# Kernel optimization log

Hardware: AMD Instinct MI355X
Metric: run time of the kernel (lower is better)

Reference implementation:

```python
import jax, jax.numpy as jnp
import numpy as np

TOP_K = 2


def setup_inputs() -> dict:
    key = jax.random.key(0)
    k1, k2, k3, k4 = jax.random.split(key, 4)
    B, S, D, F, E = 4, 512, 512, 2048, 16
    hidden_states = jax.random.normal(k1, (B, S, D), dtype=jnp.float32)
    gate_weight = jax.random.normal(k2, (E, D), dtype=jnp.float32) * 0.02
    w1 = jax.random.normal(k3, (E, F, D), dtype=jnp.float32) * 0.02
    w2 = jax.random.normal(k4, (E, D, F), dtype=jnp.float32) * 0.02
    return {"hidden_states": hidden_states, "gate_weight": gate_weight, "w1": w1, "w2": w2}


def reference(hidden_states, gate_weight, w1, w2):
    B, S, D = hidden_states.shape
    E = gate_weight.shape[0]
    x = hidden_states.reshape(-1, D)  # [T, D]

    # fused_top_k_routing: logits = x @ Wg^T, top-k, softmax over the k values
    gate_logits = x @ gate_weight.T  # [T, E]
    top_vals, top_idx = jax.lax.top_k(gate_logits, TOP_K)  # [T, k]
    routing_w = jax.nn.softmax(top_vals, axis=-1)  # [T, k]

    # _prepare_expert_inputs: token t goes to expert e iff e in its top-k
    mask = jnp.any(top_idx[:, :, None] == jnp.arange(E)[None, None, :], axis=1)  # [T, E] bool

    # Expert FFN on routed tokens, computed densely over (token, expert) pairs then masked.
    # h[t,e,f] = silu(x_t @ W1_e^T)
    h = jax.nn.silu(jnp.einsum('td,efd->tef', x, w1))  # [T, E, F]
    counts = jnp.sum(mask, axis=0)  # [E]
    h_sum = jnp.einsum('tef,te->ef', h, mask.astype(h.dtype))  # [E, F]
    h_mean = h_sum / jnp.maximum(counts, 1)[:, None].astype(h.dtype)

    # fused_expert_scatter_gather uses expert_outputs[e].mean(dim=0);
    # mean(W2 @ act) = W2 @ mean(act) since W2 is linear.
    y_mean = jnp.einsum('ef,edf->ed', h_mean, w2)  # [E, D]
    y_mean = jnp.where((counts > 0)[:, None], y_mean, 0.0)

    # per-token combine: sum_k w_k * mean_output[expert_k]
    out = jnp.einsum('tk,tkd->td', routing_w, y_mean[top_idx])  # [T, D]
    return out.reshape(B, S, D)
```

## Files before the change

kernel.cpp:

```cpp
#include <hip/hip_runtime.h>

#define NTOK   2048
#define DIM    512
#define FDIM   2048
#define NEXP   16
#define CAP    768
#define BT2    128
#define NTB    (CAP / BT2)
#define CNTS   32

typedef __bf16 bf16x8 __attribute__((ext_vector_type(8)));
typedef __bf16 bf16x4 __attribute__((ext_vector_type(4)));
typedef float  floatx4 __attribute__((ext_vector_type(4)));

#define WS_COUNTS    0
#define WS_ZEROPAGE  2048
#define WS_TOPIDX    4096
#define WS_ROUTW     20480
#define WS_HMEAN     36864
#define WS_YMEAN     167936
#define WS_XG        200704
#define WS_ZERO_BYTES 3072

__global__ __launch_bounds__(256) void k1_route_gather(
    const float* __restrict__ x, const float* __restrict__ gw,
    int* __restrict__ counts, int* __restrict__ top_idx,
    float* __restrict__ routw, __bf16* __restrict__ Xg,
    float* __restrict__ hmean)
{
    __shared__ float xt[8 * DIM];
    __shared__ float lg[8][17];
    __shared__ int   cnt_loc[16], base_loc[16];
    __shared__ int   ei[8][2], rk[8][2], gdst[8][2];
    const int tid = threadIdx.x;
    const int t0  = blockIdx.x * 8;

    if (tid < 128) hmean[blockIdx.x * 128 + tid] = 0.f;
    if (tid < 16)  cnt_loc[tid] = 0;

    {
        const float4* src = (const float4*)(x + (size_t)t0 * DIM);
        float4* dst = (float4*)xt;
        #pragma unroll
        for (int i = 0; i < 4; ++i) dst[i * 256 + tid] = src[i * 256 + tid];
    }
    __syncthreads();

    if (tid < 128) {
        const int tl = tid >> 4, e = tid & 15;
        const float4* xr = (const float4*)(xt + tl * DIM);
        const float4* gr = (const float4*)(gw + e * DIM);
        float acc = 0.f;
        #pragma unroll 8
        for (int j = 0; j < DIM / 4; ++j) {
            float4 a = xr[j], b = gr[j];
            acc += a.x * b.x + a.y * b.y + a.z * b.z + a.w * b.w;
        }
        lg[tl][e] = acc;
    }
    __syncthreads();

    if (tid < 8) {
        const int tl = tid;
        float v0 = -1e30f, v1 = -1e30f; int i0 = 0, i1 = 0;
        #pragma unroll
        for (int e = 0; e < NEXP; ++e) {
            float v = lg[tl][e];
            if (v > v0)      { v1 = v0; i1 = i0; v0 = v; i0 = e; }
            else if (v > v1) { v1 = v;  i1 = e; }
        }
        float e1 = __expf(v1 - v0);
        float w0 = 1.f / (1.f + e1);
        float w1 = 1.f - w0;
        const int t = t0 + tl;
        top_idx[t * 2]     = i0; top_idx[t * 2 + 1] = i1;
        routw[t * 2]       = w0; routw[t * 2 + 1]   = w1;
        ei[tl][0] = i0; ei[tl][1] = i1;
        rk[tl][0] = atomicAdd(&cnt_loc[i0], 1);
        rk[tl][1] = atomicAdd(&cnt_loc[i1], 1);
    }
    __syncthreads();
    if (tid < 16) {
        int n = cnt_loc[tid];
        base_loc[tid] = (n > 0) ? atomicAdd(counts + tid * CNTS, n) : 0;
    }
    __syncthreads();
    if (tid < 8) {
        #pragma unroll
        for (int k = 0; k < 2; ++k) {
            int p = base_loc[ei[tid][k]] + rk[tid][k];
            gdst[tid][k] = (p < CAP) ? (ei[tid][k] * CAP + p) : -1;
        }
    }
    __syncthreads();

    #pragma unroll
    for (int it = 0; it < 4; ++it) {
        int s   = it * 256 + tid;
        int job = s >> 6, el = s & 63;
        int tl  = job >> 1, k = job & 1;
        int dst = gdst[tl][k];
        if (dst >= 0) {
            float4 a = ((const float4*)(xt + tl * DIM))[el * 2];
            float4 b = ((const float4*)(xt + tl * DIM))[el * 2 + 1];
            bf16x8 o;
            o[0] = (__bf16)a.x; o[1] = (__bf16)a.y; o[2] = (__bf16)a.z; o[3] = (__bf16)a.w;
            o[4] = (__bf16)b.x; o[5] = (__bf16)b.y; o[6] = (__bf16)b.z; o[7] = (__bf16)b.w;
            *(bf16x8*)(Xg + (size_t)dst * DIM + el * 8) = o;
        }
    }
}

__global__ __launch_bounds__(256) void k2_expert_ffn(
    const float* __restrict__ w1, const __bf16* __restrict__ Xg,
    const int* __restrict__ counts, const __bf16* __restrict__ zp,
    float* __restrict__ hmean)
{
    __shared__ __align__(16) __bf16 w1s[8 * 65 * 8];
    __shared__ __align__(16) __bf16 xs[8 * 129 * 8];
    __shared__ float hred[64][2];

    const int tid = threadIdx.x;
    const int bid = blockIdx.x;
    const int tb  = bid >> 9;
    const int rem = bid & 511;
    const int e   = rem & 15;
    const int f0  = (rem >> 4) * 64;
    const int cnt = min(counts[e * CNTS], CAP);
    if (tb * BT2 >= cnt) return;
    const float inv = 1.f / (float)cnt;

    const int wv   = tid >> 6;
    const int lane = tid & 63;
    const int q    = lane >> 4;
    const int l15  = lane & 15;
    const int fsub = (wv & 1) * 32;
    const int tsub = (wv >> 1) * 64;

    floatx4 acc[2][4];
    #pragma unroll
    for (int a = 0; a < 2; ++a)
        #pragma unroll
        for (int b = 0; b < 4; ++b) acc[a][b] = (floatx4)0.f;

    for (int c = 0; c < 8; ++c) {
        const int d0 = c * 64;
        __syncthreads();
        #pragma unroll
        for (int it = 0; it < 2; ++it) {
            int s = it * 256 + tid;
            int f = s >> 3, g = s & 7;
            const float* src = w1 + ((size_t)(e * FDIM + f0 + f)) * DIM + d0 + g * 8;
            float4 a = ((const float4*)src)[0];
            float4 b = ((const float4*)src)[1];
            bf16x8 v;
            v[0] = (__bf16)a.x; v[1] = (__bf16)a.y; v[2] = (__bf16)a.z; v[3] = (__bf16)a.w;
            v[4] = (__bf16)b.x; v[5] = (__bf16)b.y; v[6] = (__bf16)b.z; v[7] = (__bf16)b.w;
            *(bf16x8*)(w1s + ((size_t)g * 65 + f) * 8) = v;
        }
        {
            const int kg = tid & 7;
            const int r0 = tid >> 3;
            #pragma unroll
            for (int it = 0; it < 4; ++it) {
                int t = it * 32 + r0;
                int r = tb * BT2 + t;
                const __bf16* src = (r < cnt)
                    ? (Xg + ((size_t)(e * CAP + r)) * DIM + d0 + kg * 8)
                    : zp;
                uint4 d = *(const uint4*)src;
                *(uint4*)(xs + ((size_t)kg * 129 + t) * 8) = d;
            }
        }
        __syncthreads();
        #pragma unroll
        for (int ks = 0; ks < 2; ++ks) {
            const int kg = ks * 4 + q;
            bf16x8 af0 = *(const bf16x8*)(w1s + (kg * 65 + fsub + l15) * 8);
            bf16x8 af1 = *(const bf16x8*)(w1s + (kg * 65 + fsub + 16 + l15) * 8);
            #pragma unroll
            for (int tt = 0; tt < 4; ++tt) {
                bf16x8 bfr = *(const bf16x8*)(xs + (kg * 129 + tsub + tt * 16 + l15) * 8);
                acc[0][tt] = __builtin_amdgcn_mfma_f32_16x16x32_bf16(af0, bfr, acc[0][tt], 0, 0, 0);
                acc[1][tt] = __builtin_amdgcn_mfma_f32_16x16x32_bf16(af1, bfr, acc[1][tt], 0, 0, 0);
            }
        }
    }

    float hs[8];
    #pragma unroll
    for (int i = 0; i < 8; ++i) hs[i] = 0.f;
    #pragma unroll
    for (int fa = 0; fa < 2; ++fa)
        #pragma unroll
        for (int tt = 0; tt < 4; ++tt)
            #pragma unroll
            for (int r = 0; r < 4; ++r) {
                float v = acc[fa][tt][r];
                hs[fa * 4 + r] += v / (1.f + __expf(-v));
            }

    #pragma unroll
    for (int i = 0; i < 8; ++i) {
        float v = hs[i];
        v += __shfl_xor(v, 1);
        v += __shfl_xor(v, 2);
        v += __shfl_xor(v, 4);
        v += __shfl_xor(v, 8);
        hs[i] = v;
    }
    if (l15 == 0) {
        #pragma unroll
        for (int fa = 0; fa < 2; ++fa)
            #pragma unroll
            for (int r = 0; r < 4; ++r) {
                int row = fsub + fa * 16 + q * 4 + r;
                hred[row][wv >> 1] = hs[fa * 4 + r];
            }
    }
    __syncthreads();
    if (tid < 64)
        atomicAdd(hmean + (size_t)e * FDIM + f0 + tid,
                  (hred[tid][0] + hred[tid][1]) * inv);
}

__global__ __launch_bounds__(256) void k3_ymean(
    const float* __restrict__ w2, const float* __restrict__ hmean,
    const int* __restrict__ counts, float* __restrict__ ymean)
{
    __shared__ float hl[FDIM];
    const int tid = threadIdx.x;
    const int bid = blockIdx.x;
    const int e   = bid >> 7;
    const int d0  = (bid & 127) * 4;

    {
        const float4* hg = (const float4*)(hmean + (size_t)e * FDIM);
        float4* hl4 = (float4*)hl;
        hl4[tid]       = hg[tid];
        hl4[256 + tid] = hg[256 + tid];
    }
    __syncthreads();

    const int wv = tid >> 6, lane = tid & 63;
    const int d = d0 + wv;
    const float4* wr  = (const float4*)(w2 + ((size_t)e * DIM + d) * FDIM);
    const float4* hl4 = (const float4*)hl;
    float acc = 0.f;
    #pragma unroll
    for (int i = 0; i < 8; ++i) {
        float4 a = wr[i * 64 + lane];
        float4 h = hl4[i * 64 + lane];
        acc += a.x * h.x + a.y * h.y + a.z * h.z + a.w * h.w;
    }
    #pragma unroll
    for (int m = 1; m < 64; m <<= 1) acc += __shfl_xor(acc, m);
    if (lane == 0)
        ymean[e * DIM + d] = (counts[e * CNTS] > 0) ? acc : 0.f;
}

__global__ __launch_bounds__(256) void k4_combine(
    const int* __restrict__ top_idx, const float* __restrict__ routw,
    const float* __restrict__ ymean, float* __restrict__ out)
{
    const int idx = blockIdx.x * 256 + threadIdx.x;
    const int t = idx >> 7;
    const int c = idx & 127;
    const int i0 = top_idx[t * 2], i1 = top_idx[t * 2 + 1];
    const float w0 = routw[t * 2], w1 = routw[t * 2 + 1];
    float4 a = ((const float4*)(ymean + (size_t)i0 * DIM))[c];
    float4 b = ((const float4*)(ymean + (size_t)i1 * DIM))[c];
    float4 o;
    o.x = w0 * a.x + w1 * b.x;
    o.y = w0 * a.y + w1 * b.y;
    o.z = w0 * a.z + w1 * b.z;
    o.w = w0 * a.w + w1 * b.w;
    ((float4*)out)[idx] = o;
}

extern "C" void kernel_launch(void* const* d_in, const int* in_sizes, int n_in,
                              void* d_out, int out_size, void* d_ws, size_t ws_size,
                              hipStream_t stream)
{
    (void)in_sizes; (void)n_in; (void)out_size; (void)ws_size;
    const float* x  = (const float*)d_in[0];
    const float* gw = (const float*)d_in[1];
    const float* w1 = (const float*)d_in[2];
    const float* w2 = (const float*)d_in[3];
    float* out = (float*)d_out;

    char* ws = (char*)d_ws;
    int*    counts  = (int*)   (ws + WS_COUNTS);
    const __bf16* zp = (const __bf16*)(ws + WS_ZEROPAGE);
    int*    top_idx = (int*)   (ws + WS_TOPIDX);
    float*  routw   = (float*) (ws + WS_ROUTW);
    float*  hmean   = (float*) (ws + WS_HMEAN);
    float*  ymean   = (float*) (ws + WS_YMEAN);
    __bf16* Xg      = (__bf16*)(ws + WS_XG);

    hipMemsetAsync(d_ws, 0, WS_ZERO_BYTES, stream);

    k1_route_gather<<<dim3(NTOK / 8), dim3(256), 0, stream>>>(x, gw, counts, top_idx, routw, Xg, hmean);
    k2_expert_ffn  <<<dim3(NTB * 32 * NEXP), dim3(256), 0, stream>>>(w1, Xg, counts, zp, hmean);
    k3_ymean       <<<dim3(NEXP * 128), dim3(256), 0, stream>>>(w2, hmean, counts, ymean);
    k4_combine     <<<dim3(NTOK * DIM / 4 / 256), dim3(256), 0, stream>>>(top_idx, routw, ymean, out);
}
```

Measured before the change: 198.6 us.

## Fuse four MoE kernels into one persistent kernel with grid barriers

Merges routing/gather, expert FFN, W2 projection and combine into a single 512-block persistent kernel separated by software grid barriers on a workspace counter. Each FFN block now loops over all token tiles of its expert and writes hmean directly, so the atomics and the separate hmean zeroing go away. This removes three kernel launch gaps and inter-kernel drains. In exchange it relies on all 512 blocks being co-resident (two per CU) and serializes token tiles per block, which cuts the FFN stage's parallelism.

```diff
diff --git a/kernel.cpp b/kernel.cpp
--- a/kernel.cpp
+++ b/kernel.cpp
@@ -6,14 +6,14 @@
 #define NEXP   16
 #define CAP    768
 #define BT2    128
-#define NTB    (CAP / BT2)
 #define CNTS   32
+#define NBLK   512
 
 typedef __bf16 bf16x8 __attribute__((ext_vector_type(8)));
-typedef __bf16 bf16x4 __attribute__((ext_vector_type(4)));
 typedef float  floatx4 __attribute__((ext_vector_type(4)));
 
 #define WS_COUNTS    0
+#define WS_BAR       64
 #define WS_ZEROPAGE  2048
 #define WS_TOPIDX    4096
 #define WS_ROUTW     20480
@@ -22,260 +22,271 @@
 #define WS_XG        200704
 #define WS_ZERO_BYTES 3072
 
-__global__ __launch_bounds__(256) void k1_route_gather(
+__device__ __forceinline__ void grid_bar(int* bar, int target) {
+    __syncthreads();
+    if (threadIdx.x == 0) {
+        __threadfence();
+        __hip_atomic_fetch_add(bar, 1, __ATOMIC_RELEASE, __HIP_MEMORY_SCOPE_AGENT);
+        while (__hip_atomic_load(bar, __ATOMIC_ACQUIRE, __HIP_MEMORY_SCOPE_AGENT) < target)
+            __builtin_amdgcn_s_sleep(2);
+    }
+    __syncthreads();
+    __threadfence();
+}
+
+__global__ __launch_bounds__(256, 2) void fused_moe(
     const float* __restrict__ x, const float* __restrict__ gw,
-    int* __restrict__ counts, int* __restrict__ top_idx,
-    float* __restrict__ routw, __bf16* __restrict__ Xg,
-    float* __restrict__ hmean)
+    const float* __restrict__ w1, const float* __restrict__ w2,
+    int* counts, int* bar, int* top_idx, float* routw, __bf16* Xg,
+    const __bf16* zp, float* hmean, float* ymean, float* out)
 {
-    __shared__ float xt[8 * DIM];
-    __shared__ float lg[8][17];
-    __shared__ int   cnt_loc[16], base_loc[16];
-    __shared__ int   ei[8][2], rk[8][2], gdst[8][2];
-    const int tid = threadIdx.x;
-    const int t0  = blockIdx.x * 8;
-
-    if (tid < 128) hmean[blockIdx.x * 128 + tid] = 0.f;
-    if (tid < 16)  cnt_loc[tid] = 0;
-
-    {
-        const float4* src = (const float4*)(x + (size_t)t0 * DIM);
-        float4* dst = (float4*)xt;
-        #pragma unroll
-        for (int i = 0; i < 4; ++i) dst[i * 256 + tid] = src[i * 256 + tid];
-    }
-    __syncthreads();
-
-    if (tid < 128) {
-        const int tl = tid >> 4, e = tid & 15;
-        const float4* xr = (const float4*)(xt + tl * DIM);
-        const float4* gr = (const float4*)(gw + e * DIM);
-        float acc = 0.f;
-        #pragma unroll 8
-        for (int j = 0; j < DIM / 4; ++j) {
-            float4 a = xr[j], b = gr[j];
-            acc += a.x * b.x + a.y * b.y + a.z * b.z + a.w * b.w;
-        }
-        lg[tl][e] = acc;
-    }
-    __syncthreads();
-
-    if (tid < 8) {
-        const int tl = tid;
-        float v0 = -1e30f, v1 = -1e30f; int i0 = 0, i1 = 0;
-        #pragma unroll
-        for (int e = 0; e < NEXP; ++e) {
-            float v = lg[tl][e];
-            if (v > v0)      { v1 = v0; i1 = i0; v0 = v; i0 = e; }
-            else if (v > v1) { v1 = v;  i1 = e; }
-        }
-        float e1 = __expf(v1 - v0);
-        float w0 = 1.f / (1.f + e1);
-        float w1 = 1.f - w0;
-        const int t = t0 + tl;
-        top_idx[t * 2]     = i0; top_idx[t * 2 + 1] = i1;
-        routw[t * 2]       = w0; routw[t * 2 + 1]   = w1;
-        ei[tl][0] = i0; ei[tl][1] = i1;
-        rk[tl][0] = atomicAdd(&cnt_loc[i0], 1);
-        rk[tl][1] = atomicAdd(&cnt_loc[i1], 1);
-    }
-    __syncthreads();
-    if (tid < 16) {
-        int n = cnt_loc[tid];
-        base_loc[tid] = (n > 0) ? atomicAdd(counts + tid * CNTS, n) : 0;
-    }
-    __syncthreads();
-    if (tid < 8) {
-        #pragma unroll
-        for (int k = 0; k < 2; ++k) {
-            int p = base_loc[ei[tid][k]] + rk[tid][k];
-            gdst[tid][k] = (p < CAP) ? (ei[tid][k] * CAP + p) : -1;
-        }
-    }
-    __syncthreads();
-
-    #pragma unroll
-    for (int it = 0; it < 4; ++it) {
-        int s   = it * 256 + tid;
-        int job = s >> 6, el = s & 63;
-        int tl  = job >> 1, k = job & 1;
-        int dst = gdst[tl][k];
-        if (dst >= 0) {
-            float4 a = ((const float4*)(xt + tl * DIM))[el * 2];
-            float4 b = ((const float4*)(xt + tl * DIM))[el * 2 + 1];
-            bf16x8 o;
-            o[0] = (__bf16)a.x; o[1] = (__bf16)a.y; o[2] = (__bf16)a.z; o[3] = (__bf16)a.w;
-            o[4] = (__bf16)b.x; o[5] = (__bf16)b.y; o[6] = (__bf16)b.z; o[7] = (__bf16)b.w;
-            *(bf16x8*)(Xg + (size_t)dst * DIM + el * 8) = o;
-        }
-    }
-}
-
-__global__ __launch_bounds__(256) void k2_expert_ffn(
-    const float* __restrict__ w1, const __bf16* __restrict__ Xg,
-    const int* __restrict__ counts, const __bf16* __restrict__ zp,
-    float* __restrict__ hmean)
-{
-    __shared__ __align__(16) __bf16 w1s[8 * 65 * 8];
-    __shared__ __align__(16) __bf16 xs[8 * 129 * 8];
-    __shared__ float hred[64][2];
-
+    __shared__ __align__(16) char smem[25600];
     const int tid = threadIdx.x;
     const int bid = blockIdx.x;
-    const int tb  = bid >> 9;
-    const int rem = bid & 511;
-    const int e   = rem & 15;
-    const int f0  = (rem >> 4) * 64;
-    const int cnt = min(counts[e * CNTS], CAP);
-    if (tb * BT2 >= cnt) return;
-    const float inv = 1.f / (float)cnt;
-
-    const int wv   = tid >> 6;
-    const int lane = tid & 63;
-    const int q    = lane >> 4;
-    const int l15  = lane & 15;
-    const int fsub = (wv & 1) * 32;
-    const int tsub = (wv >> 1) * 64;
-
-    floatx4 acc[2][4];
-    #pragma unroll
-    for (int a = 0; a < 2; ++a)
-        #pragma unroll
-        for (int b = 0; b < 4; ++b) acc[a][b] = (floatx4)0.f;
-
-    for (int c = 0; c < 8; ++c) {
-        const int d0 = c * 64;
-        __syncthreads();
+
+    {
+        float* xt        = (float*)smem;
+        float (*lg)[17]  = (float(*)[17])(smem + 8192);
+        int*   cnt_loc   = (int*)(smem + 8464);
+        int*   base_loc  = (int*)(smem + 8528);
+        int   (*ei)[2]   = (int(*)[2])(smem + 8592);
+        int   (*rk)[2]   = (int(*)[2])(smem + 8624);
+        int   (*gdst)[2] = (int(*)[2])(smem + 8656);
+        const int t0 = bid * 4;
+
+        if (tid < 16) cnt_loc[tid] = 0;
+        {
+            const float4* src = (const float4*)(x + (size_t)t0 * DIM);
+            float4* dst = (float4*)xt;
+            #pragma unroll
+            for (int i = 0; i < 2; ++i) dst[i * 256 + tid] = src[i * 256 + tid];
+        }
+        __syncthreads();
+
+        if (tid < 64) {
+            const int tl = tid >> 4, e = tid & 15;
+            const float4* xr = (const float4*)(xt + tl * DIM);
+            const float4* gr = (const float4*)(gw + e * DIM);
+            float acc = 0.f;
+            #pragma unroll 8
+            for (int j = 0; j < DIM / 4; ++j) {
+                float4 a = xr[j], b = gr[j];
+                acc += a.x * b.x + a.y * b.y + a.z * b.z + a.w * b.w;
+            }
+            lg[tl][e] = acc;
+        }
+        __syncthreads();
+
+        if (tid < 4) {
+            const int tl = tid;
+            float v0 = -1e30f, v1 = -1e30f; int i0 = 0, i1 = 0;
+            #pragma unroll
+            for (int e = 0; e < NEXP; ++e) {
+                float v = lg[tl][e];
+                if (v > v0)      { v1 = v0; i1 = i0; v0 = v; i0 = e; }
+                else if (v > v1) { v1 = v;  i1 = e; }
+            }
+            float e1 = __expf(v1 - v0);
+            float w0 = 1.f / (1.f + e1);
+            float w1v = 1.f - w0;
+            const int t = t0 + tl;
+            top_idx[t * 2]     = i0; top_idx[t * 2 + 1] = i1;
+            routw[t * 2]       = w0; routw[t * 2 + 1]   = w1v;
+            ei[tl][0] = i0; ei[tl][1] = i1;
+            rk[tl][0] = atomicAdd(&cnt_loc[i0], 1);
+            rk[tl][1] = atomicAdd(&cnt_loc[i1], 1);
+        }
+        __syncthreads();
+        if (tid < 16) {
+            int n = cnt_loc[tid];
+            base_loc[tid] = (n > 0) ? atomicAdd(counts + tid * CNTS, n) : 0;
+        }
+        __syncthreads();
+        if (tid < 4) {
+            #pragma unroll
+            for (int k = 0; k < 2; ++k) {
+                int p = base_loc[ei[tid][k]] + rk[tid][k];
+                gdst[tid][k] = (p < CAP) ? (ei[tid][k] * CAP + p) : -1;
+            }
+        }
+        __syncthreads();
+
         #pragma unroll
         for (int it = 0; it < 2; ++it) {
-            int s = it * 256 + tid;
-            int f = s >> 3, g = s & 7;
-            const float* src = w1 + ((size_t)(e * FDIM + f0 + f)) * DIM + d0 + g * 8;
-            float4 a = ((const float4*)src)[0];
-            float4 b = ((const float4*)src)[1];
-            bf16x8 v;
-            v[0] = (__bf16)a.x; v[1] = (__bf16)a.y; v[2] = (__bf16)a.z; v[3] = (__bf16)a.w;
-            v[4] = (__bf16)b.x; v[5] = (__bf16)b.y; v[6] = (__bf16)b.z; v[7] = (__bf16)b.w;
-            *(bf16x8*)(w1s + ((size_t)g * 65 + f) * 8) = v;
-        }
+            int s   = it * 256 + tid;
+            int job = s >> 6, el = s & 63;
+            int tl  = job >> 1, k = job & 1;
+            int dst = gdst[tl][k];
+            if (dst >= 0) {
+                float4 a = ((const float4*)(xt + tl * DIM))[el * 2];
+                float4 b = ((const float4*)(xt + tl * DIM))[el * 2 + 1];
+                bf16x8 o;
+                o[0] = (__bf16)a.x; o[1] = (__bf16)a.y; o[2] = (__bf16)a.z; o[3] = (__bf16)a.w;
+                o[4] = (__bf16)b.x; o[5] = (__bf16)b.y; o[6] = (__bf16)b.z; o[7] = (__bf16)b.w;
+                *(bf16x8*)(Xg + (size_t)dst * DIM + el * 8) = o;
+            }
+        }
+    }
+    grid_bar(bar, NBLK);
+
+    {
+        __bf16* w1s = (__bf16*)smem;
+        __bf16* xs  = (__bf16*)(smem + 8320);
+        float (*hred)[2] = (float(*)[2])(smem + 24832);
+
+        const int e   = bid & 15;
+        const int f0  = (bid >> 4) * 64;
+        const int cnt = min(counts[e * CNTS], CAP);
+        const float inv = 1.f / (float)max(cnt, 1);
+
+        const int wv   = tid >> 6;
+        const int lane = tid & 63;
+        const int q    = lane >> 4;
+        const int l15  = lane & 15;
+        const int fsub = (wv & 1) * 32;
+        const int tsub = (wv >> 1) * 64;
+
+        float hs[8];
+        #pragma unroll
+        for (int i = 0; i < 8; ++i) hs[i] = 0.f;
+
+        for (int tb = 0; tb * BT2 < cnt; ++tb) {
+            floatx4 acc[2][4];
+            #pragma unroll
+            for (int a = 0; a < 2; ++a)
+                #pragma unroll
+                for (int b = 0; b < 4; ++b) acc[a][b] = (floatx4)0.f;
+
+            for (int c = 0; c < 8; ++c) {
+                const int d0 = c * 64;
+                __syncthreads();
+                #pragma unroll
+                for (int it = 0; it < 2; ++it) {
+                    int ss = it * 256 + tid;
+                    int f = ss >> 3, g = ss & 7;
+                    const float* src = w1 + ((size_t)(e * FDIM + f0 + f)) * DIM + d0 + g * 8;
+                    float4 a = ((const float4*)src)[0];
+                    float4 b = ((const float4*)src)[1];
+                    bf16x8 v;
+                    v[0] = (__bf16)a.x; v[1] = (__bf16)a.y; v[2] = (__bf16)a.z; v[3] = (__bf16)a.w;
+                    v[4] = (__bf16)b.x; v[5] = (__bf16)b.y; v[6] = (__bf16)b.z; v[7] = (__bf16)b.w;
+                    *(bf16x8*)(w1s + ((size_t)g * 65 + f) * 8) = v;
+                }
+                {
+                    const int kg = tid & 7;
+                    const int r0 = tid >> 3;
+                    #pragma unroll
+                    for (int it = 0; it < 4; ++it) {
+                        int t = it * 32 + r0;
+                        int r = tb * BT2 + t;
+                        const __bf16* src = (r < cnt)
+                            ? (Xg + ((size_t)(e * CAP + r)) * DIM + d0 + kg * 8)
+                            : zp;
+                        uint4 d = *(const uint4*)src;
+                        *(uint4*)(xs + ((size_t)kg * 129 + t) * 8) = d;
+                    }
+                }
+                __syncthreads();
+                #pragma unroll
+                for (int ks = 0; ks < 2; ++ks) {
+                    const int kg = ks * 4 + q;
+                    bf16x8 af0 = *(const bf16x8*)(w1s + (kg * 65 + fsub + l15) * 8);
+                    bf16x8 af1 = *(const bf16x8*)(w1s + (kg * 65 + fsub + 16 + l15) * 8);
+                    #pragma unroll
+                    for (int tt = 0; tt < 4; ++tt) {
+                        bf16x8 bfr = *(const bf16x8*)(xs + (kg * 129 + tsub + tt * 16 + l15) * 8);
+                        acc[0][tt] = __builtin_amdgcn_mfma_f32_16x16x32_bf16(af0, bfr, acc[0][tt], 0, 0, 0);
+                        acc[1][tt] = __builtin_amdgcn_mfma_f32_16x16x32_bf16(af1, bfr, acc[1][tt], 0, 0, 0);
+                    }
+                }
+            }
+
+            #pragma unroll
+            for (int fa = 0; fa < 2; ++fa)
+                #pragma unroll
+                for (int tt = 0; tt < 4; ++tt)
+                    #pragma unroll
+                    for (int r = 0; r < 4; ++r) {
+                        float v = acc[fa][tt][r];
+                        hs[fa * 4 + r] += v / (1.f + __expf(-v));
+                    }
+        }
+
+        #pragma unroll
+        for (int i = 0; i < 8; ++i) {
+            float v = hs[i];
+            v += __shfl_xor(v, 1);
+            v += __shfl_xor(v, 2);
+            v += __shfl_xor(v, 4);
+            v += __shfl_xor(v, 8);
+            hs[i] = v;
+        }
+        if (l15 == 0) {
+            #pragma unroll
+            for (int fa = 0; fa < 2; ++fa)
+                #pragma unroll
+                for (int r = 0; r < 4; ++r) {
+                    int row = fsub + fa * 16 + q * 4 + r;
+                    hred[row][wv >> 1] = hs[fa * 4 + r];
+                }
+        }
+        __syncthreads();
+        if (tid < 64)
+            hmean[(size_t)e * FDIM + f0 + tid] =
+                (hred[tid][0] + hred[tid][1]) * inv;
+    }
+    grid_bar(bar, 2 * NBLK);
+
+    {
+        float* hl = (float*)smem;
+        const int e  = bid >> 5;
+        const int d0 = (bid & 31) * 16;
         {
-            const int kg = tid & 7;
-            const int r0 = tid >> 3;
-            #pragma unroll
-            for (int it = 0; it < 4; ++it) {
-                int t = it * 32 + r0;
-                int r = tb * BT2 + t;
-                const __bf16* src = (r < cnt)
-                    ? (Xg + ((size_t)(e * CAP + r)) * DIM + d0 + kg * 8)
-                    : zp;
-                uint4 d = *(const uint4*)src;
-                *(uint4*)(xs + ((size_t)kg * 129 + t) * 8) = d;
-            }
-        }
-        __syncthreads();
+            const float4* hg = (const float4*)(hmean + (size_t)e * FDIM);
+            float4* hl4 = (float4*)hl;
+            hl4[tid]       = hg[tid];
+            hl4[256 + tid] = hg[256 + tid];
+        }
+        __syncthreads();
+
+        const int wv = tid >> 6, lane = tid & 63;
+        const float4* hl4 = (const float4*)hl;
+        const int live = (counts[e * CNTS] > 0);
         #pragma unroll
-        for (int ks = 0; ks < 2; ++ks) {
-            const int kg = ks * 4 + q;
-            bf16x8 af0 = *(const bf16x8*)(w1s + (kg * 65 + fsub + l15) * 8);
-            bf16x8 af1 = *(const bf16x8*)(w1s + (kg * 65 + fsub + 16 + l15) * 8);
-            #pragma unroll
-            for (int tt = 0; tt < 4; ++tt) {
-                bf16x8 bfr = *(const bf16x8*)(xs + (kg * 129 + tsub + tt * 16 + l15) * 8);
-                acc[0][tt] = __builtin_amdgcn_mfma_f32_16x16x32_bf16(af0, bfr, acc[0][tt], 0, 0, 0);
-                acc[1][tt] = __builtin_amdgcn_mfma_f32_16x16x32_bf16(af1, bfr, acc[1][tt], 0, 0, 0);
-            }
-        }
-    }
-
-    float hs[8];
+        for (int j = 0; j < 4; ++j) {
+            const int d = d0 + j * 4 + wv;
+            const float4* wr = (const float4*)(w2 + ((size_t)e * DIM + d) * FDIM);
+            float acc = 0.f;
+            #pragma unroll
+            for (int i = 0; i < 8; ++i) {
+                float4 a = wr[i * 64 + lane];
+                float4 h = hl4[i * 64 + lane];
+                acc += a.x * h.x + a.y * h.y + a.z * h.z + a.w * h.w;
+            }
+            #pragma unroll
+            for (int m = 1; m < 64; m <<= 1) acc += __shfl_xor(acc, m);
+            if (lane == 0)
+                ymean[e * DIM + d] = live ? acc : 0.f;
+        }
+    }
+    grid_bar(bar, 3 * NBLK);
+
     #pragma unroll
-    for (int i = 0; i < 8; ++i) hs[i] = 0.f;
-    #pragma unroll
-    for (int fa = 0; fa < 2; ++fa)
-        #pragma unroll
-        for (int tt = 0; tt < 4; ++tt)
-            #pragma unroll
-            for (int r = 0; r < 4; ++r) {
-                float v = acc[fa][tt][r];
-                hs[fa * 4 + r] += v / (1.f + __expf(-v));
-            }
-
-    #pragma unroll
-    for (int i = 0; i < 8; ++i) {
-        float v = hs[i];
-        v += __shfl_xor(v, 1);
-        v += __shfl_xor(v, 2);
-        v += __shfl_xor(v, 4);
-        v += __shfl_xor(v, 8);
-        hs[i] = v;
-    }
-    if (l15 == 0) {
-        #pragma unroll
-        for (int fa = 0; fa < 2; ++fa)
-            #pragma unroll
-            for (int r = 0; r < 4; ++r) {
-                int row = fsub + fa * 16 + q * 4 + r;
-                hred[row][wv >> 1] = hs[fa * 4 + r];
-            }
-    }
-    __syncthreads();
-    if (tid < 64)
-        atomicAdd(hmean + (size_t)e * FDIM + f0 + tid,
-                  (hred[tid][0] + hred[tid][1]) * inv);
-}
-
-__global__ __launch_bounds__(256) void k3_ymean(
-    const float* __restrict__ w2, const float* __restrict__ hmean,
-    const int* __restrict__ counts, float* __restrict__ ymean)
-{
-    __shared__ float hl[FDIM];
-    const int tid = threadIdx.x;
-    const int bid = blockIdx.x;
-    const int e   = bid >> 7;
-    const int d0  = (bid & 127) * 4;
-
-    {
-        const float4* hg = (const float4*)(hmean + (size_t)e * FDIM);
-        float4* hl4 = (float4*)hl;
-        hl4[tid]       = hg[tid];
-        hl4[256 + tid] = hg[256 + tid];
-    }
-    __syncthreads();
-
-    const int wv = tid >> 6, lane = tid & 63;
-    const int d = d0 + wv;
-    const float4* wr  = (const float4*)(w2 + ((size_t)e * DIM + d) * FDIM);
-    const float4* hl4 = (const float4*)hl;
-    float acc = 0.f;
-    #pragma unroll
-    for (int i = 0; i < 8; ++i) {
-        float4 a = wr[i * 64 + lane];
-        float4 h = hl4[i * 64 + lane];
-        acc += a.x * h.x + a.y * h.y + a.z * h.z + a.w * h.w;
-    }
-    #pragma unroll
-    for (int m = 1; m < 64; m <<= 1) acc += __shfl_xor(acc, m);
-    if (lane == 0)
-        ymean[e * DIM + d] = (counts[e * CNTS] > 0) ? acc : 0.f;
-}
-
-__global__ __launch_bounds__(256) void k4_combine(
-    const int* __restrict__ top_idx, const float* __restrict__ routw,
-    const float* __restrict__ ymean, float* __restrict__ out)
-{
-    const int idx = blockIdx.x * 256 + threadIdx.x;
-    const int t = idx >> 7;
-    const int c = idx & 127;
-    const int i0 = top_idx[t * 2], i1 = top_idx[t * 2 + 1];
-    const float w0 = routw[t * 2], w1 = routw[t * 2 + 1];
-    float4 a = ((const float4*)(ymean + (size_t)i0 * DIM))[c];
-    float4 b = ((const float4*)(ymean + (size_t)i1 * DIM))[c];
-    float4 o;
-    o.x = w0 * a.x + w1 * b.x;
-    o.y = w0 * a.y + w1 * b.y;
-    o.z = w0 * a.z + w1 * b.z;
-    o.w = w0 * a.w + w1 * b.w;
-    ((float4*)out)[idx] = o;
+    for (int it = 0; it < 2; ++it) {
+        const int idx = bid * 512 + it * 256 + tid;
+        const int t = idx >> 7;
+        const int c = idx & 127;
+        const int i0 = top_idx[t * 2], i1 = top_idx[t * 2 + 1];
+        const float w0 = routw[t * 2], w1v = routw[t * 2 + 1];
+        float4 a = ((const float4*)(ymean + (size_t)i0 * DIM))[c];
+        float4 b = ((const float4*)(ymean + (size_t)i1 * DIM))[c];
+        float4 o;
+        o.x = w0 * a.x + w1v * b.x;
+        o.y = w0 * a.y + w1v * b.y;
+        o.z = w0 * a.z + w1v * b.z;
+        o.w = w0 * a.w + w1v * b.w;
+        ((float4*)out)[idx] = o;
+    }
 }
 
 extern "C" void kernel_launch(void* const* d_in, const int* in_sizes, int n_in,
@@ -291,6 +302,7 @@
 
     char* ws = (char*)d_ws;
     int*    counts  = (int*)   (ws + WS_COUNTS);
+    int*    bar     = (int*)   (ws + WS_BAR);
     const __bf16* zp = (const __bf16*)(ws + WS_ZEROPAGE);
     int*    top_idx = (int*)   (ws + WS_TOPIDX);
     float*  routw   = (float*) (ws + WS_ROUTW);
@@ -300,8 +312,6 @@
 
     hipMemsetAsync(d_ws, 0, WS_ZERO_BYTES, stream);
 
-    k1_route_gather<<<dim3(NTOK / 8), dim3(256), 0, stream>>>(x, gw, counts, top_idx, routw, Xg, hmean);
-    k2_expert_ffn  <<<dim3(NTB * 32 * NEXP), dim3(256), 0, stream>>>(w1, Xg, counts, zp, hmean);
-    k3_ymean       <<<dim3(NEXP * 128), dim3(256), 0, stream>>>(w2, hmean, counts, ymean);
-    k4_combine     <<<dim3(NTOK * DIM / 4 / 256), dim3(256), 0, stream>>>(top_idx, routw, ymean, out);
+    fused_moe<<<dim3(NBLK), dim3(256), 0, stream>>>(
+        x, gw, w1, w2, counts, bar, top_idx, routw, Xg, zp, hmean, ymean, out);
 }
```

Result: slower. 476.3 us (+139.8%).
